# Kernel optimization log

Hardware: AMD Instinct MI355X
Metric: run time of the kernel (lower is better)

## Reference

```python
import jax, jax.numpy as jnp
import numpy as np

EPS = 1e-5  # torch BatchNorm default eps, eval mode with running stats

def _bn(x, g, b, m, v):
    shp = (1, -1) + (1,) * (x.ndim - 2)
    return (x - m.reshape(shp)) * (g.reshape(shp) / jnp.sqrt(v.reshape(shp) + EPS)) + b.reshape(shp)

def _lrelu(x):
    return jnp.where(x > 0, x, 0.2 * x)

def setup_inputs() -> dict:
    key = jax.random.key(0)
    ks = jax.random.split(key, 20)
    B, N, K = 4, 2048, 32
    Cin, Cf, Co = 6, 64, 64  # in_channels, feat_channels, out_channels(==nhiddens)
    f32 = jnp.float32
    def randn(k, shape, s=1.0):
        return jax.random.normal(k, shape, f32) * s
    def bnp(k, c):
        k1, k2, k3, k4 = jax.random.split(k, 4)
        return (randn(k1, (c,)), randn(k2, (c,)), randn(k3, (c,), 0.1),
                jax.random.uniform(k4, (c,), f32, 0.5, 1.5))
    inp = {
        "x": randn(ks[0], (B, Cin, N, K)),          # knn_points
        "y": randn(ks[1], (B, Cf, N, K)),           # knn_feat
        "points": randn(ks[2], (B, Cin // 2, N)),
        "feat": randn(ks[3], (B, Cf // 2, N)),
        "Wq": randn(ks[4], (Cf, Cf // 2), 0.1),
        "Wpos1": randn(ks[5], (Cin, Cin // 2), 0.1),
        "Wpos2": randn(ks[6], (Cf, Cin), 0.1),
        "Wattn": randn(ks[7], (Co * Cin, Cf), 0.1),
        "Wlin": randn(ks[8], (Co, Co), 0.1),
        "Wres": randn(ks[9], (Co, Cf), 0.1),
    }
    for name, k, c in [("q", ks[10], Cf), ("p", ks[11], Cin), ("a", ks[12], Co * Cin),
                       ("1", ks[13], Co), ("l", ks[14], Co), ("r", ks[15], Co)]:
        g, b, m, v = bnp(k, c)
        inp["g" + name], inp["b" + name], inp["m" + name], inp["v" + name] = g, b, m, v
    return inp

def reference(x, y, points, feat, Wq, Wpos1, Wpos2, Wattn, Wlin, Wres,
              gq, bq, mq, vq, gp, bp, mp, vp, ga, ba, ma, va,
              g1, b1, m1, v1, gl, bl, ml, vl, gr, br, mr, vr):
    B, Cin, N, K = x.shape
    Cf = y.shape[1]
    Co = Wattn.shape[0] // Cin
    # query projection (conv1d 1x1 == per-point GEMM) + BN + LeakyReLU
    x_q = _lrelu(_bn(jnp.einsum('oi,bin->bon', Wq, feat), gq, bq, mq, vq))   # [B,Cf,N]
    # positional branch
    pos = _lrelu(_bn(jnp.einsum('oi,bin->bon', Wpos1, points), gp, bp, mp, vp))  # [B,Cin,N]
    pos = pos[:, :, :, None] - x                                             # [B,Cin,N,K]
    pos = jnp.einsum('oi,bink->bonk', Wpos2, pos)                            # [B,Cf,N,K]
    # vector (subtraction) attention, softmax over neighbors k
    attn = x_q[:, :, :, None] - y + pos                                      # [B,Cf,N,K]
    attn = jax.nn.softmax(attn / float(np.sqrt(Cf)), axis=-1)
    attn = _bn(jnp.einsum('oi,bink->bonk', Wattn, attn), ga, ba, ma, va)     # [B,Co*Cin,N,K]
    # per-point tiny matmul: [Co,Cin] @ [Cin] for every (b,n,k)
    attn = attn.transpose(0, 2, 3, 1).reshape(B, N, K, Co, Cin)
    out = jnp.einsum('bnkoi,bnki->bonk', attn, x.transpose(0, 2, 3, 1))      # [B,Co,N,K]
    h = _lrelu(_bn(out, g1, b1, m1, v1))
    h = _bn(jnp.einsum('oi,bink->bonk', Wlin, h), gl, bl, ml, vl)
    res = _bn(jnp.einsum('oi,bink->bonk', Wres, y), gr, br, mr, vr)
    return _lrelu(h + res)
```

## Files before the change

### kernel.cpp

```cpp
#include <hip/hip_runtime.h>

constexpr int NB  = 4;
constexpr int NPT = 2048;
constexpr int KNN = 32;
constexpr int CIN = 6;
constexpr int CF  = 64;
constexpr int CO  = 64;
constexpr float EPS = 1e-5f;

typedef short bf16x8 __attribute__((ext_vector_type(8)));
typedef float f32x4  __attribute__((ext_vector_type(4)));

constexpr size_t WS_WA  = 0;
constexpr size_t WS_WL  = 49152;
constexpr size_t WS_WR  = 57344;
constexpr size_t WS_BA  = 65536;
constexpr size_t WS_BNF = 67072;

__device__ __host__ inline unsigned short bf16_rne(float f) {
  unsigned u = __builtin_bit_cast(unsigned, f);
  u += 0x7fffu + ((u >> 16) & 1u);
  return (unsigned short)(u >> 16);
}

__global__ void setup_kernel(const float *Wattn, const float *Wlin, const float *Wres,
                             const float *ga, const float *ba, const float *ma, const float *va,
                             const float *g1, const float *b1, const float *m1, const float *v1,
                             const float *gl, const float *bl, const float *ml, const float *vl,
                             const float *gr, const float *br, const float *mr, const float *vr,
                             unsigned short *WAf, unsigned short *WLf, unsigned short *WRf,
                             float *baP, float *bnf) {
  const int t = blockIdx.x * blockDim.x + threadIdx.x;
  const int stride = gridDim.x * blockDim.x;
  for (int e = t; e < 6 * 4 * 2 * 64 * 8; e += stride) {
    const int j = e & 7, l = (e >> 3) & 63, ks = (e >> 9) & 1, ot = (e >> 10) & 3, i = e >> 12;
    const int m = l & 15, cg = l >> 4;
    const int cc = ks * 32 + cg * 8 + j;
    const int row = (ot * 16 + m) * CIN + i;
    const float sa = ga[row] * rsqrtf(va[row] + EPS);
    WAf[e] = bf16_rne(Wattn[row * CF + cc] * sa);
  }
  for (int e = t; e < 4 * 2 * 64 * 8; e += stride) {
    const int j = e & 7, l = (e >> 3) & 63, ks = (e >> 9) & 1, ot = e >> 10;
    const int m = l & 15;
    const int cc = ks * 32 + (l >> 4) * 8 + j;
    const int row = ot * 16 + m;
    const float sl = gl[row] * rsqrtf(vl[row] + EPS);
    const float sr = gr[row] * rsqrtf(vr[row] + EPS);
    WLf[e] = bf16_rne(Wlin[row * CF + cc] * sl);
    WRf[e] = bf16_rne(Wres[row * CF + cc] * sr);
  }
  for (int e = t; e < 384; e += stride) {
    const int i = e >> 6, o = e & 63;
    const int j0 = o * CIN + i;
    const float sa = ga[j0] * rsqrtf(va[j0] + EPS);
    baP[e] = ba[j0] - ma[j0] * sa;
  }
  for (int e = t; e < 64; e += stride) {
    const float s1v = g1[e] * rsqrtf(v1[e] + EPS);
    bnf[e]      = s1v;
    bnf[64 + e] = b1[e] - m1[e] * s1v;
    const float slv = gl[e] * rsqrtf(vl[e] + EPS);
    const float srv = gr[e] * rsqrtf(vr[e] + EPS);
    bnf[128 + e] = (bl[e] - ml[e] * slv) + (br[e] - mr[e] * srv);
  }
}

struct Params {
  const float *x, *y, *points, *feat;
  const float *Wq, *Wpos1, *Wpos2;
  const float *gq, *bq, *mq, *vq;
  const float *gp, *bp, *mp, *vp;
  const unsigned short *WAf, *WLf, *WRf;
  const float *baP, *bnf;
  float *out;
};

__global__ __launch_bounds__(256) void fused_pt_attn(Params p) {
  const int tid  = threadIdx.x;
  const int lane = tid & 63;
  const int wid  = tid >> 6;
  const int bid  = ((blockIdx.x & 7) << 8) + (blockIdx.x >> 3);
  const int pidx = bid * 4 + wid;
  const int b    = pidx >> 11;
  const int n    = pidx & (NPT - 1);

  __shared__ unsigned short s_B[4][2 * 2048];
  __shared__ float s_d[4][192];
  __shared__ float s_f[4][32];
  unsigned short *yB = s_B[wid];
  unsigned short *PB = s_B[wid] + 2048;
  float *dW = s_d[wid];
  float *fW = s_f[wid];

  float ftv = 0.f, ptv = 0.f;
  if (lane < 32) ftv = p.feat[((size_t)b * 32 + lane) * NPT + n];
  if (lane < 3)  ptv = p.points[((size_t)b * 3 + lane) * NPT + n];
  const int xi = lane >> 3, xk = (lane & 7) * 4;
  float4 x4 = make_float4(0.f, 0.f, 0.f, 0.f);
  if (lane < 48)
    x4 = *(const float4 *)(p.x + (((size_t)b * CIN + xi) * NPT + n) * KNN + xk);
  const float *w2p = p.Wpos2 + lane * 6;
  const float2 w2a = *(const float2 *)(w2p);
  const float2 w2b = *(const float2 *)(w2p + 2);
  const float2 w2c = *(const float2 *)(w2p + 4);
  const float w2[6] = {w2a.x, w2a.y, w2b.x, w2b.y, w2c.x, w2c.y};

  if (lane < 32) fW[lane] = ftv;

  const float pt0 = __shfl(ptv, 0), pt1 = __shfl(ptv, 1), pt2 = __shfl(ptv, 2);
  float pos1[6];
#pragma unroll
  for (int i = 0; i < 6; ++i) {
    const float a = p.Wpos1[i * 3 + 0] * pt0 + p.Wpos1[i * 3 + 1] * pt1 +
                    p.Wpos1[i * 3 + 2] * pt2;
    const float s = p.gp[i] * rsqrtf(p.vp[i] + EPS);
    const float v = fmaf(a, s, p.bp[i] - p.mp[i] * s);
    pos1[i] = v > 0.f ? v : 0.2f * v;
  }

  if (lane < 48) {
    float pi = pos1[0];
    pi = (xi == 1) ? pos1[1] : pi;
    pi = (xi == 2) ? pos1[2] : pi;
    pi = (xi == 3) ? pos1[3] : pi;
    pi = (xi == 4) ? pos1[4] : pi;
    pi = (xi == 5) ? pos1[5] : pi;
    *(float4 *)(dW + xi * 32 + xk) =
        make_float4(pi - x4.x, pi - x4.y, pi - x4.z, pi - x4.w);
  }

  float xq;
  {
    float acc = 0.f;
    const float *wq = p.Wq + lane * 32;
#pragma unroll
    for (int q = 0; q < 8; ++q) {
      const float4 w4 = *(const float4 *)(wq + q * 4);
      const float4 f4 = *(const float4 *)(fW + q * 4);
      acc = fmaf(w4.x, f4.x, fmaf(w4.y, f4.y, fmaf(w4.z, f4.z, fmaf(w4.w, f4.w, acc))));
    }
    const float s = p.gq[lane] * rsqrtf(p.vq[lane] + EPS);
    const float v = fmaf(acc, s, p.bq[lane] - p.mq[lane] * s);
    xq = v > 0.f ? v : 0.2f * v;
  }

  float pre[32];
#pragma unroll
  for (int k = 0; k < 32; ++k) pre[k] = 0.f;
#pragma unroll
  for (int i = 0; i < 6; ++i) {
    const float wv = w2[i];
#pragma unroll
    for (int q = 0; q < 8; ++q) {
      const float4 d4 = *(const float4 *)(dW + i * 32 + q * 4);
      pre[q * 4 + 0] = fmaf(wv, d4.x, pre[q * 4 + 0]);
      pre[q * 4 + 1] = fmaf(wv, d4.y, pre[q * 4 + 1]);
      pre[q * 4 + 2] = fmaf(wv, d4.z, pre[q * 4 + 2]);
      pre[q * 4 + 3] = fmaf(wv, d4.w, pre[q * 4 + 3]);
    }
  }

  const float *yrow = p.y + (((size_t)b * CF + lane) * NPT + n) * KNN;
#pragma unroll
  for (int q = 0; q < 8; ++q) {
    const float4 y4 = *(const float4 *)(yrow + q * 4);
    const float yv[4] = {y4.x, y4.y, y4.z, y4.w};
#pragma unroll
    for (int j = 0; j < 4; ++j) {
      const int k = q * 4 + j;
      yB[k * 64 + (lane ^ ((k & 7) << 3))] = bf16_rne(yv[j]);
      pre[k] = (xq - yv[j] + pre[k]) * 0.125f;
    }
  }

  float mx = pre[0];
#pragma unroll
  for (int k = 1; k < 32; ++k) mx = fmaxf(mx, pre[k]);
  float sum = 0.f;
#pragma unroll
  for (int k = 0; k < 32; ++k) { pre[k] = __expf(pre[k] - mx); sum += pre[k]; }
  const float inv = 1.f / sum;
#pragma unroll
  for (int k = 0; k < 32; ++k)
    PB[k * 64 + (lane ^ ((k & 7) << 3))] = bf16_rne(pre[k] * inv);

  const int og = lane >> 4, kl = lane & 15;

  float xvv[6][2];
#pragma unroll
  for (int i = 0; i < 6; ++i)
#pragma unroll
    for (int nt = 0; nt < 2; ++nt)
      xvv[i][nt] = pos1[i] - dW[i * 32 + kl + nt * 16];

  bf16x8 Ba[2][2];
#pragma unroll
  for (int ks = 0; ks < 2; ++ks)
#pragma unroll
    for (int nt = 0; nt < 2; ++nt) {
      const int kcol = kl + nt * 16;
      Ba[ks][nt] = *(const bf16x8 *)(PB + kcol * 64 + ((ks * 32 + og * 8) ^ ((kcol & 7) << 3)));
    }

  const bf16x8 *WAv = (const bf16x8 *)p.WAf;
#pragma unroll
  for (int ot = 0; ot < 4; ++ot) {
    float out1[2][4] = {{0.f, 0.f, 0.f, 0.f}, {0.f, 0.f, 0.f, 0.f}};
#pragma unroll
    for (int i = 0; i < 6; ++i) {
      const bf16x8 A0 = WAv[((i * 4 + ot) * 2 + 0) * 64 + lane];
      const bf16x8 A1 = WAv[((i * 4 + ot) * 2 + 1) * 64 + lane];
      const f32x4 ba4 = *(const f32x4 *)(p.baP + i * 64 + ot * 16 + og * 4);
#pragma unroll
      for (int nt = 0; nt < 2; ++nt) {
        f32x4 g = {0.f, 0.f, 0.f, 0.f};
        g = __builtin_amdgcn_mfma_f32_16x16x32_bf16(A0, Ba[0][nt], g, 0, 0, 0);
        g = __builtin_amdgcn_mfma_f32_16x16x32_bf16(A1, Ba[1][nt], g, 0, 0, 0);
        const float xv = xvv[i][nt];
#pragma unroll
        for (int r = 0; r < 4; ++r)
          out1[nt][r] = fmaf(g[r] + ba4[r], xv, out1[nt][r]);
      }
    }
    const f32x4 s14 = *(const f32x4 *)(p.bnf + 0 * 64 + ot * 16 + og * 4);
    const f32x4 b14 = *(const f32x4 *)(p.bnf + 1 * 64 + ot * 16 + og * 4);
#pragma unroll
    for (int nt = 0; nt < 2; ++nt) {
      const int kcol = kl + nt * 16;
      unsigned hp[4];
#pragma unroll
      for (int r = 0; r < 4; ++r) {
        const float t = fmaf(s14[r], out1[nt][r], b14[r]);
        hp[r] = bf16_rne(t > 0.f ? t : 0.2f * t);
      }
      const int idx = kcol * 64 + ((ot * 16 + og * 4) ^ ((kcol & 7) << 3));
      *(uint2 *)(PB + idx) = make_uint2(hp[0] | (hp[1] << 16), hp[2] | (hp[3] << 16));
    }
  }

  bf16x8 Bh[2][2], By[2][2];
#pragma unroll
  for (int ks = 0; ks < 2; ++ks)
#pragma unroll
    for (int nt = 0; nt < 2; ++nt) {
      const int kcol = kl + nt * 16;
      const int off = kcol * 64 + ((ks * 32 + og * 8) ^ ((kcol & 7) << 3));
      Bh[ks][nt] = *(const bf16x8 *)(PB + off);
      By[ks][nt] = *(const bf16x8 *)(yB + off);
    }
  const bf16x8 *WLv = (const bf16x8 *)p.WLf;
  const bf16x8 *WRv = (const bf16x8 *)p.WRf;
#pragma unroll
  for (int ot = 0; ot < 4; ++ot) {
    const bf16x8 L0 = WLv[(ot * 2 + 0) * 64 + lane];
    const bf16x8 L1 = WLv[(ot * 2 + 1) * 64 + lane];
    const bf16x8 R0 = WRv[(ot * 2 + 0) * 64 + lane];
    const bf16x8 R1 = WRv[(ot * 2 + 1) * 64 + lane];
    const f32x4 blr = *(const f32x4 *)(p.bnf + 2 * 64 + ot * 16 + og * 4);
#pragma unroll
    for (int nt = 0; nt < 2; ++nt) {
      f32x4 a = {0.f, 0.f, 0.f, 0.f};
      a = __builtin_amdgcn_mfma_f32_16x16x32_bf16(L0, Bh[0][nt], a, 0, 0, 0);
      a = __builtin_amdgcn_mfma_f32_16x16x32_bf16(L1, Bh[1][nt], a, 0, 0, 0);
      a = __builtin_amdgcn_mfma_f32_16x16x32_bf16(R0, By[0][nt], a, 0, 0, 0);
      a = __builtin_amdgcn_mfma_f32_16x16x32_bf16(R1, By[1][nt], a, 0, 0, 0);
      const int kcol = kl + nt * 16;
      float *ob = p.out + (((size_t)(b * CO + ot * 16 + og * 4)) * NPT + n) * KNN + kcol;
#pragma unroll
      for (int r = 0; r < 4; ++r) {
        const float v = a[r] + blr[r];
        ob[(size_t)r * NPT * KNN] = v > 0.f ? v : 0.2f * v;
      }
    }
  }
}

extern "C" void kernel_launch(void *const *d_in, const int *in_sizes, int n_in,
                              void *d_out, int out_size, void *d_ws, size_t ws_size,
                              hipStream_t stream) {
  char *ws = (char *)d_ws;
  unsigned short *WAf = (unsigned short *)(ws + WS_WA);
  unsigned short *WLf = (unsigned short *)(ws + WS_WL);
  unsigned short *WRf = (unsigned short *)(ws + WS_WR);
  float *baP = (float *)(ws + WS_BA);
  float *bnf = (float *)(ws + WS_BNF);

  setup_kernel<<<dim3(96), dim3(256), 0, stream>>>(
      (const float *)d_in[7], (const float *)d_in[8], (const float *)d_in[9],
      (const float *)d_in[18], (const float *)d_in[19], (const float *)d_in[20], (const float *)d_in[21],
      (const float *)d_in[22], (const float *)d_in[23], (const float *)d_in[24], (const float *)d_in[25],
      (const float *)d_in[26], (const float *)d_in[27], (const float *)d_in[28], (const float *)d_in[29],
      (const float *)d_in[30], (const float *)d_in[31], (const float *)d_in[32], (const float *)d_in[33],
      WAf, WLf, WRf, baP, bnf);

  Params p;
  p.x      = (const float *)d_in[0];
  p.y      = (const float *)d_in[1];
  p.points = (const float *)d_in[2];
  p.feat   = (const float *)d_in[3];
  p.Wq     = (const float *)d_in[4];
  p.Wpos1  = (const float *)d_in[5];
  p.Wpos2  = (const float *)d_in[6];
  p.gq = (const float *)d_in[10]; p.bq = (const float *)d_in[11];
  p.mq = (const float *)d_in[12]; p.vq = (const float *)d_in[13];
  p.gp = (const float *)d_in[14]; p.bp = (const float *)d_in[15];
  p.mp = (const float *)d_in[16]; p.vp = (const float *)d_in[17];
  p.WAf = WAf; p.WLf = WLf; p.WRf = WRf;
  p.baP = baP; p.bnf = bnf;
  p.out = (float *)d_out;

  fused_pt_attn<<<dim3(NB * NPT / 4), dim3(256), 0, stream>>>(p);
}
```

Baseline: 66.88 us.

## Process two points per wavefront to reuse weight fragments across MFMAs

Each wavefront now handles two adjacent points instead of one, halving the grid and sharing the WA/WL/WR MFMA A-fragments and bias loads between both points. Global loads for x, y, feat and points are widened to cover both points, and y and softmax probabilities share one LDS buffer per point, with the softmax written after the y fragments are read back. It also packs the per-point x differences into bf16 pairs and sets launch_bounds occupancy to 4. Register pressure roughly doubles, and bf16 rounding of the x multiplier adds precision loss.

```diff
diff --git a/kernel.cpp b/kernel.cpp
--- a/kernel.cpp
+++ b/kernel.cpp
@@ -76,179 +76,246 @@
   float *out;
 };
 
-__global__ __launch_bounds__(256) void fused_pt_attn(Params p) {
+__global__ __launch_bounds__(256, 4) void fused_pt_attn(Params p) {
   const int tid  = threadIdx.x;
   const int lane = tid & 63;
   const int wid  = tid >> 6;
-  const int bid  = ((blockIdx.x & 7) << 8) + (blockIdx.x >> 3);
-  const int pidx = bid * 4 + wid;
-  const int b    = pidx >> 11;
-  const int n    = pidx & (NPT - 1);
-
-  __shared__ unsigned short s_B[4][2 * 2048];
-  __shared__ float s_d[4][192];
-  __shared__ float s_f[4][32];
-  unsigned short *yB = s_B[wid];
-  unsigned short *PB = s_B[wid] + 2048;
-  float *dW = s_d[wid];
-  float *fW = s_f[wid];
-
-  float ftv = 0.f, ptv = 0.f;
-  if (lane < 32) ftv = p.feat[((size_t)b * 32 + lane) * NPT + n];
-  if (lane < 3)  ptv = p.points[((size_t)b * 3 + lane) * NPT + n];
+  const int bid  = ((blockIdx.x & 7) << 7) | (blockIdx.x >> 3);
+  const int pb   = (bid * 4 + wid) * 2;
+  const int b    = pb >> 11;
+  const int n0   = pb & (NPT - 1);
+
+  __shared__ unsigned short s_BB[4][2][2048];
+  __shared__ float s_d[4][2][192];
+  __shared__ float s_f[4][2][32];
+  unsigned short *BB0 = s_BB[wid][0], *BB1 = s_BB[wid][1];
+  float *dW0 = s_d[wid][0], *dW1 = s_d[wid][1];
+  float *fW0 = s_f[wid][0], *fW1 = s_f[wid][1];
+
+  float2 ft2 = make_float2(0.f, 0.f), pt2 = make_float2(0.f, 0.f);
+  if (lane < 32) ft2 = *(const float2 *)(p.feat + ((size_t)b * 32 + lane) * NPT + n0);
+  if (lane < 3)  pt2 = *(const float2 *)(p.points + ((size_t)b * 3 + lane) * NPT + n0);
   const int xi = lane >> 3, xk = (lane & 7) * 4;
-  float4 x4 = make_float4(0.f, 0.f, 0.f, 0.f);
-  if (lane < 48)
-    x4 = *(const float4 *)(p.x + (((size_t)b * CIN + xi) * NPT + n) * KNN + xk);
+  float4 x40 = make_float4(0.f, 0.f, 0.f, 0.f), x41 = x40;
+  if (lane < 48) {
+    const float *xb = p.x + (((size_t)b * CIN + xi) * NPT + n0) * KNN + xk;
+    x40 = *(const float4 *)(xb);
+    x41 = *(const float4 *)(xb + KNN);
+  }
   const float *w2p = p.Wpos2 + lane * 6;
   const float2 w2a = *(const float2 *)(w2p);
   const float2 w2b = *(const float2 *)(w2p + 2);
   const float2 w2c = *(const float2 *)(w2p + 4);
   const float w2[6] = {w2a.x, w2a.y, w2b.x, w2b.y, w2c.x, w2c.y};
 
-  if (lane < 32) fW[lane] = ftv;
-
-  const float pt0 = __shfl(ptv, 0), pt1 = __shfl(ptv, 1), pt2 = __shfl(ptv, 2);
-  float pos1[6];
+  if (lane < 32) { fW0[lane] = ft2.x; fW1[lane] = ft2.y; }
+
+  const float pA0 = __shfl(pt2.x, 0), pA1 = __shfl(pt2.x, 1), pA2 = __shfl(pt2.x, 2);
+  const float pB0 = __shfl(pt2.y, 0), pB1 = __shfl(pt2.y, 1), pB2 = __shfl(pt2.y, 2);
+  float pos10[6], pos11[6];
 #pragma unroll
   for (int i = 0; i < 6; ++i) {
-    const float a = p.Wpos1[i * 3 + 0] * pt0 + p.Wpos1[i * 3 + 1] * pt1 +
-                    p.Wpos1[i * 3 + 2] * pt2;
-    const float s = p.gp[i] * rsqrtf(p.vp[i] + EPS);
-    const float v = fmaf(a, s, p.bp[i] - p.mp[i] * s);
-    pos1[i] = v > 0.f ? v : 0.2f * v;
+    const float w0 = p.Wpos1[i * 3 + 0], w1 = p.Wpos1[i * 3 + 1], wv = p.Wpos1[i * 3 + 2];
+    const float s  = p.gp[i] * rsqrtf(p.vp[i] + EPS);
+    const float bb = p.bp[i] - p.mp[i] * s;
+    float a0 = fmaf(w0, pA0, fmaf(w1, pA1, wv * pA2));
+    a0 = fmaf(a0, s, bb);
+    pos10[i] = a0 > 0.f ? a0 : 0.2f * a0;
+    float a1 = fmaf(w0, pB0, fmaf(w1, pB1, wv * pB2));
+    a1 = fmaf(a1, s, bb);
+    pos11[i] = a1 > 0.f ? a1 : 0.2f * a1;
   }
 
   if (lane < 48) {
-    float pi = pos1[0];
-    pi = (xi == 1) ? pos1[1] : pi;
-    pi = (xi == 2) ? pos1[2] : pi;
-    pi = (xi == 3) ? pos1[3] : pi;
-    pi = (xi == 4) ? pos1[4] : pi;
-    pi = (xi == 5) ? pos1[5] : pi;
-    *(float4 *)(dW + xi * 32 + xk) =
-        make_float4(pi - x4.x, pi - x4.y, pi - x4.z, pi - x4.w);
-  }
-
-  float xq;
+    float pi0 = pos10[0], pi1 = pos11[0];
+    pi0 = (xi == 1) ? pos10[1] : pi0;  pi1 = (xi == 1) ? pos11[1] : pi1;
+    pi0 = (xi == 2) ? pos10[2] : pi0;  pi1 = (xi == 2) ? pos11[2] : pi1;
+    pi0 = (xi == 3) ? pos10[3] : pi0;  pi1 = (xi == 3) ? pos11[3] : pi1;
+    pi0 = (xi == 4) ? pos10[4] : pi0;  pi1 = (xi == 4) ? pos11[4] : pi1;
+    pi0 = (xi == 5) ? pos10[5] : pi0;  pi1 = (xi == 5) ? pos11[5] : pi1;
+    *(float4 *)(dW0 + xi * 32 + xk) = make_float4(pi0 - x40.x, pi0 - x40.y, pi0 - x40.z, pi0 - x40.w);
+    *(float4 *)(dW1 + xi * 32 + xk) = make_float4(pi1 - x41.x, pi1 - x41.y, pi1 - x41.z, pi1 - x41.w);
+  }
+
+  float xq0, xq1;
   {
-    float acc = 0.f;
+    float a0 = 0.f, a1 = 0.f;
     const float *wq = p.Wq + lane * 32;
 #pragma unroll
     for (int q = 0; q < 8; ++q) {
       const float4 w4 = *(const float4 *)(wq + q * 4);
-      const float4 f4 = *(const float4 *)(fW + q * 4);
-      acc = fmaf(w4.x, f4.x, fmaf(w4.y, f4.y, fmaf(w4.z, f4.z, fmaf(w4.w, f4.w, acc))));
-    }
-    const float s = p.gq[lane] * rsqrtf(p.vq[lane] + EPS);
-    const float v = fmaf(acc, s, p.bq[lane] - p.mq[lane] * s);
-    xq = v > 0.f ? v : 0.2f * v;
-  }
-
-  float pre[32];
-#pragma unroll
-  for (int k = 0; k < 32; ++k) pre[k] = 0.f;
+      const float4 f0 = *(const float4 *)(fW0 + q * 4);
+      const float4 f1 = *(const float4 *)(fW1 + q * 4);
+      a0 = fmaf(w4.x, f0.x, fmaf(w4.y, f0.y, fmaf(w4.z, f0.z, fmaf(w4.w, f0.w, a0))));
+      a1 = fmaf(w4.x, f1.x, fmaf(w4.y, f1.y, fmaf(w4.z, f1.z, fmaf(w4.w, f1.w, a1))));
+    }
+    const float s  = p.gq[lane] * rsqrtf(p.vq[lane] + EPS);
+    const float bb = p.bq[lane] - p.mq[lane] * s;
+    const float v0 = fmaf(a0, s, bb), v1 = fmaf(a1, s, bb);
+    xq0 = v0 > 0.f ? v0 : 0.2f * v0;
+    xq1 = v1 > 0.f ? v1 : 0.2f * v1;
+  }
+
+  float pre0[32], pre1[32];
+#pragma unroll
+  for (int k = 0; k < 32; ++k) { pre0[k] = 0.f; pre1[k] = 0.f; }
 #pragma unroll
   for (int i = 0; i < 6; ++i) {
     const float wv = w2[i];
 #pragma unroll
     for (int q = 0; q < 8; ++q) {
-      const float4 d4 = *(const float4 *)(dW + i * 32 + q * 4);
-      pre[q * 4 + 0] = fmaf(wv, d4.x, pre[q * 4 + 0]);
-      pre[q * 4 + 1] = fmaf(wv, d4.y, pre[q * 4 + 1]);
-      pre[q * 4 + 2] = fmaf(wv, d4.z, pre[q * 4 + 2]);
-      pre[q * 4 + 3] = fmaf(wv, d4.w, pre[q * 4 + 3]);
-    }
-  }
-
-  const float *yrow = p.y + (((size_t)b * CF + lane) * NPT + n) * KNN;
+      const float4 d0 = *(const float4 *)(dW0 + i * 32 + q * 4);
+      const float4 d1 = *(const float4 *)(dW1 + i * 32 + q * 4);
+      pre0[q * 4 + 0] = fmaf(wv, d0.x, pre0[q * 4 + 0]);
+      pre0[q * 4 + 1] = fmaf(wv, d0.y, pre0[q * 4 + 1]);
+      pre0[q * 4 + 2] = fmaf(wv, d0.z, pre0[q * 4 + 2]);
+      pre0[q * 4 + 3] = fmaf(wv, d0.w, pre0[q * 4 + 3]);
+      pre1[q * 4 + 0] = fmaf(wv, d1.x, pre1[q * 4 + 0]);
+      pre1[q * 4 + 1] = fmaf(wv, d1.y, pre1[q * 4 + 1]);
+      pre1[q * 4 + 2] = fmaf(wv, d1.z, pre1[q * 4 + 2]);
+      pre1[q * 4 + 3] = fmaf(wv, d1.w, pre1[q * 4 + 3]);
+    }
+  }
+
+  const float *yrow0 = p.y + (((size_t)b * CF + lane) * NPT + n0) * KNN;
 #pragma unroll
   for (int q = 0; q < 8; ++q) {
-    const float4 y4 = *(const float4 *)(yrow + q * 4);
-    const float yv[4] = {y4.x, y4.y, y4.z, y4.w};
+    const float4 y0 = *(const float4 *)(yrow0 + q * 4);
+    const float4 y1 = *(const float4 *)(yrow0 + KNN + q * 4);
+    const float yv0[4] = {y0.x, y0.y, y0.z, y0.w};
+    const float yv1[4] = {y1.x, y1.y, y1.z, y1.w};
 #pragma unroll
     for (int j = 0; j < 4; ++j) {
       const int k = q * 4 + j;
-      yB[k * 64 + (lane ^ ((k & 7) << 3))] = bf16_rne(yv[j]);
-      pre[k] = (xq - yv[j] + pre[k]) * 0.125f;
-    }
-  }
-
-  float mx = pre[0];
-#pragma unroll
-  for (int k = 1; k < 32; ++k) mx = fmaxf(mx, pre[k]);
-  float sum = 0.f;
-#pragma unroll
-  for (int k = 0; k < 32; ++k) { pre[k] = __expf(pre[k] - mx); sum += pre[k]; }
-  const float inv = 1.f / sum;
-#pragma unroll
-  for (int k = 0; k < 32; ++k)
-    PB[k * 64 + (lane ^ ((k & 7) << 3))] = bf16_rne(pre[k] * inv);
+      const int idx = k * 64 + (lane ^ ((k & 7) << 3));
+      BB0[idx] = bf16_rne(yv0[j]);
+      BB1[idx] = bf16_rne(yv1[j]);
+      pre0[k] = (xq0 - yv0[j] + pre0[k]) * 0.125f;
+      pre1[k] = (xq1 - yv1[j] + pre1[k]) * 0.125f;
+    }
+  }
 
   const int og = lane >> 4, kl = lane & 15;
 
-  float xvv[6][2];
-#pragma unroll
-  for (int i = 0; i < 6; ++i)
-#pragma unroll
-    for (int nt = 0; nt < 2; ++nt)
-      xvv[i][nt] = pos1[i] - dW[i * 32 + kl + nt * 16];
-
-  bf16x8 Ba[2][2];
+  bf16x8 By0[2][2], By1[2][2];
 #pragma unroll
   for (int ks = 0; ks < 2; ++ks)
 #pragma unroll
     for (int nt = 0; nt < 2; ++nt) {
       const int kcol = kl + nt * 16;
-      Ba[ks][nt] = *(const bf16x8 *)(PB + kcol * 64 + ((ks * 32 + og * 8) ^ ((kcol & 7) << 3)));
-    }
+      const int off = kcol * 64 + ((ks * 32 + og * 8) ^ ((kl & 7) << 3));
+      By0[ks][nt] = *(const bf16x8 *)(BB0 + off);
+      By1[ks][nt] = *(const bf16x8 *)(BB1 + off);
+    }
+
+  {
+    float mx0 = pre0[0], mx1 = pre1[0];
+#pragma unroll
+    for (int k = 1; k < 32; ++k) { mx0 = fmaxf(mx0, pre0[k]); mx1 = fmaxf(mx1, pre1[k]); }
+    float s0 = 0.f, s1 = 0.f;
+#pragma unroll
+    for (int k = 0; k < 32; ++k) {
+      pre0[k] = __expf(pre0[k] - mx0); s0 += pre0[k];
+      pre1[k] = __expf(pre1[k] - mx1); s1 += pre1[k];
+    }
+    const float i0 = 1.f / s0, i1 = 1.f / s1;
+#pragma unroll
+    for (int k = 0; k < 32; ++k) {
+      const int idx = k * 64 + (lane ^ ((k & 7) << 3));
+      BB0[idx] = bf16_rne(pre0[k] * i0);
+      BB1[idx] = bf16_rne(pre1[k] * i1);
+    }
+  }
+
+  bf16x8 Ba0[2][2], Ba1[2][2];
+#pragma unroll
+  for (int ks = 0; ks < 2; ++ks)
+#pragma unroll
+    for (int nt = 0; nt < 2; ++nt) {
+      const int kcol = kl + nt * 16;
+      const int off = kcol * 64 + ((ks * 32 + og * 8) ^ ((kl & 7) << 3));
+      Ba0[ks][nt] = *(const bf16x8 *)(BB0 + off);
+      Ba1[ks][nt] = *(const bf16x8 *)(BB1 + off);
+    }
+
+  unsigned xvp0[6], xvp1[6];
+#pragma unroll
+  for (int i = 0; i < 6; ++i) {
+    const float a0 = pos10[i] - dW0[i * 32 + kl];
+    const float c0 = pos10[i] - dW0[i * 32 + kl + 16];
+    const float a1 = pos11[i] - dW1[i * 32 + kl];
+    const float c1 = pos11[i] - dW1[i * 32 + kl + 16];
+    xvp0[i] = (unsigned)bf16_rne(a0) | ((unsigned)bf16_rne(c0) << 16);
+    xvp1[i] = (unsigned)bf16_rne(a1) | ((unsigned)bf16_rne(c1) << 16);
+  }
 
   const bf16x8 *WAv = (const bf16x8 *)p.WAf;
 #pragma unroll
   for (int ot = 0; ot < 4; ++ot) {
-    float out1[2][4] = {{0.f, 0.f, 0.f, 0.f}, {0.f, 0.f, 0.f, 0.f}};
+    f32x4 o00 = {0.f, 0.f, 0.f, 0.f}, o01 = o00, o10 = o00, o11 = o00;
 #pragma unroll
     for (int i = 0; i < 6; ++i) {
       const bf16x8 A0 = WAv[((i * 4 + ot) * 2 + 0) * 64 + lane];
       const bf16x8 A1 = WAv[((i * 4 + ot) * 2 + 1) * 64 + lane];
       const f32x4 ba4 = *(const f32x4 *)(p.baP + i * 64 + ot * 16 + og * 4);
-#pragma unroll
-      for (int nt = 0; nt < 2; ++nt) {
-        f32x4 g = {0.f, 0.f, 0.f, 0.f};
-        g = __builtin_amdgcn_mfma_f32_16x16x32_bf16(A0, Ba[0][nt], g, 0, 0, 0);
-        g = __builtin_amdgcn_mfma_f32_16x16x32_bf16(A1, Ba[1][nt], g, 0, 0, 0);
-        const float xv = xvv[i][nt];
-#pragma unroll
-        for (int r = 0; r < 4; ++r)
-          out1[nt][r] = fmaf(g[r] + ba4[r], xv, out1[nt][r]);
-      }
+      const float xv00 = __builtin_bit_cast(float, xvp0[i] << 16);
+      const float xv01 = __builtin_bit_cast(float, xvp0[i] & 0xffff0000u);
+      const float xv10 = __builtin_bit_cast(float, xvp1[i] << 16);
+      const float xv11 = __builtin_bit_cast(float, xvp1[i] & 0xffff0000u);
+      f32x4 g;
+      g = (f32x4){0.f, 0.f, 0.f, 0.f};
+      g = __builtin_amdgcn_mfma_f32_16x16x32_bf16(A0, Ba0[0][0], g, 0, 0, 0);
+      g = __builtin_amdgcn_mfma_f32_16x16x32_bf16(A1, Ba0[1][0], g, 0, 0, 0);
+#pragma unroll
+      for (int r = 0; r < 4; ++r) o00[r] = fmaf(g[r] + ba4[r], xv00, o00[r]);
+      g = (f32x4){0.f, 0.f, 0.f, 0.f};
+      g = __builtin_amdgcn_mfma_f32_16x16x32_bf16(A0, Ba0[0][1], g, 0, 0, 0);
+      g = __builtin_amdgcn_mfma_f32_16x16x32_bf16(A1, Ba0[1][1], g, 0, 0, 0);
+#pragma unroll
+      for (int r = 0; r < 4; ++r) o01[r] = fmaf(g[r] + ba4[r], xv01, o01[r]);
+      g = (f32x4){0.f, 0.f, 0.f, 0.f};
+      g = __builtin_amdgcn_mfma_f32_16x16x32_bf16(A0, Ba1[0][0], g, 0, 0, 0);
+      g = __builtin_amdgcn_mfma_f32_16x16x32_bf16(A1, Ba1[1][0], g, 0, 0, 0);
+#pragma unroll
+      for (int r = 0; r < 4; ++r) o10[r] = fmaf(g[r] + ba4[r], xv10, o10[r]);
+      g = (f32x4){0.f, 0.f, 0.f, 0.f};
+      g = __builtin_amdgcn_mfma_f32_16x16x32_bf16(A0, Ba1[0][1], g, 0, 0, 0);
+      g = __builtin_amdgcn_mfma_f32_16x16x32_bf16(A1, Ba1[1][1], g, 0, 0, 0);
+#pragma unroll
+      for (int r = 0; r < 4; ++r) o11[r] = fmaf(g[r] + ba4[r], xv11, o11[r]);
     }
     const f32x4 s14 = *(const f32x4 *)(p.bnf + 0 * 64 + ot * 16 + og * 4);
     const f32x4 b14 = *(const f32x4 *)(p.bnf + 1 * 64 + ot * 16 + og * 4);
 #pragma unroll
     for (int nt = 0; nt < 2; ++nt) {
       const int kcol = kl + nt * 16;
-      unsigned hp[4];
+      const int idx = kcol * 64 + ((ot * 16 + og * 4) ^ ((kl & 7) << 3));
+      const f32x4 &q0 = nt ? o01 : o00;
+      const f32x4 &q1 = nt ? o11 : o10;
+      unsigned h0[4], h1[4];
 #pragma unroll
       for (int r = 0; r < 4; ++r) {
-        const float t = fmaf(s14[r], out1[nt][r], b14[r]);
-        hp[r] = bf16_rne(t > 0.f ? t : 0.2f * t);
+        const float t0 = fmaf(s14[r], q0[r], b14[r]);
+        const float t1 = fmaf(s14[r], q1[r], b14[r]);
+        h0[r] = bf16_rne(t0 > 0.f ? t0 : 0.2f * t0);
+        h1[r] = bf16_rne(t1 > 0.f ? t1 : 0.2f * t1);
       }
-      const int idx = kcol * 64 + ((ot * 16 + og * 4) ^ ((kcol & 7) << 3));
-      *(uint2 *)(PB + idx) = make_uint2(hp[0] | (hp[1] << 16), hp[2] | (hp[3] << 16));
-    }
-  }
-
-  bf16x8 Bh[2][2], By[2][2];
+      *(uint2 *)(BB0 + idx) = make_uint2(h0[0] | (h0[1] << 16), h0[2] | (h0[3] << 16));
+      *(uint2 *)(BB1 + idx) = make_uint2(h1[0] | (h1[1] << 16), h1[2] | (h1[3] << 16));
+    }
+  }
+
+  bf16x8 Bh0[2][2], Bh1[2][2];
 #pragma unroll
   for (int ks = 0; ks < 2; ++ks)
 #pragma unroll
     for (int nt = 0; nt < 2; ++nt) {
       const int kcol = kl + nt * 16;
-      const int off = kcol * 64 + ((ks * 32 + og * 8) ^ ((kcol & 7) << 3));
-      Bh[ks][nt] = *(const bf16x8 *)(PB + off);
-      By[ks][nt] = *(const bf16x8 *)(yB + off);
-    }
+      const int off = kcol * 64 + ((ks * 32 + og * 8) ^ ((kl & 7) << 3));
+      Bh0[ks][nt] = *(const bf16x8 *)(BB0 + off);
+      Bh1[ks][nt] = *(const bf16x8 *)(BB1 + off);
+    }
+
   const bf16x8 *WLv = (const bf16x8 *)p.WLf;
   const bf16x8 *WRv = (const bf16x8 *)p.WRf;
 #pragma unroll
@@ -260,17 +327,23 @@
     const f32x4 blr = *(const f32x4 *)(p.bnf + 2 * 64 + ot * 16 + og * 4);
 #pragma unroll
     for (int nt = 0; nt < 2; ++nt) {
-      f32x4 a = {0.f, 0.f, 0.f, 0.f};
-      a = __builtin_amdgcn_mfma_f32_16x16x32_bf16(L0, Bh[0][nt], a, 0, 0, 0);
-      a = __builtin_amdgcn_mfma_f32_16x16x32_bf16(L1, Bh[1][nt], a, 0, 0, 0);
-      a = __builtin_amdgcn_mfma_f32_16x16x32_bf16(R0, By[0][nt], a, 0, 0, 0);
-      a = __builtin_amdgcn_mfma_f32_16x16x32_bf16(R1, By[1][nt], a, 0, 0, 0);
-      const int kcol = kl + nt * 16;
-      float *ob = p.out + (((size_t)(b * CO + ot * 16 + og * 4)) * NPT + n) * KNN + kcol;
+      f32x4 a0 = {0.f, 0.f, 0.f, 0.f}, a1 = a0;
+      a0 = __builtin_amdgcn_mfma_f32_16x16x32_bf16(L0, Bh0[0][nt], a0, 0, 0, 0);
+      a0 = __builtin_amdgcn_mfma_f32_16x16x32_bf16(L1, Bh0[1][nt], a0, 0, 0, 0);
+      a0 = __builtin_amdgcn_mfma_f32_16x16x32_bf16(R0, By0[0][nt], a0, 0, 0, 0);
+      a0 = __builtin_amdgcn_mfma_f32_16x16x32_bf16(R1, By0[1][nt], a0, 0, 0, 0);
+      a1 = __builtin_amdgcn_mfma_f32_16x16x32_bf16(L0, Bh1[0][nt], a1, 0, 0, 0);
+      a1 = __builtin_amdgcn_mfma_f32_16x16x32_bf16(L1, Bh1[1][nt], a1, 0, 0, 0);
+      a1 = __builtin_amdgcn_mfma_f32_16x16x32_bf16(R0, By1[0][nt], a1, 0, 0, 0);
+      a1 = __builtin_amdgcn_mfma_f32_16x16x32_bf16(R1, By1[1][nt], a1, 0, 0, 0);
+      const int kcol = kl + nt * 16;
+      float *ob = p.out + (((size_t)(b * CO + ot * 16 + og * 4)) * NPT + n0) * KNN + kcol;
 #pragma unroll
       for (int r = 0; r < 4; ++r) {
-        const float v = a[r] + blr[r];
-        ob[(size_t)r * NPT * KNN] = v > 0.f ? v : 0.2f * v;
+        const float v0 = a0[r] + blr[r];
+        const float v1 = a1[r] + blr[r];
+        ob[(size_t)r * NPT * KNN]       = v0 > 0.f ? v0 : 0.2f * v0;
+        ob[(size_t)r * NPT * KNN + KNN] = v1 > 0.f ? v1 : 0.2f * v1;
       }
     }
   }
@@ -310,5 +383,5 @@
   p.baP = baP; p.bnf = bnf;
   p.out = (float *)d_out;
 
-  fused_pt_attn<<<dim3(NB * NPT / 4), dim3(256), 0, stream>>>(p);
+  fused_pt_attn<<<dim3(NB * NPT / 8), dim3(256), 0, stream>>>(p);
 }
```

Result: slower. 119.0 us (+78.0%).

## Split output-channel tiles across waves and keep attention weights in registers

Applied to the files above, without the earlier changes.

Each block now handles 8 points in two iterations. Instead of every wave computing all 64 output channels for its own point, each wave owns one 16-channel tile and loops over the four points staged in shared memory. This lets each wave hold its slice of the large attention weight matrix in registers once, rather than reloading all of it from global memory per point. The cost is several block-wide barriers per iteration, cross-wave shared-memory traffic, extra shared arrays for x, and higher register pressure with a launch-bounds occupancy hint.

```diff
diff --git a/kernel.cpp b/kernel.cpp
--- a/kernel.cpp
+++ b/kernel.cpp
@@ -76,201 +76,230 @@
   float *out;
 };
 
-__global__ __launch_bounds__(256) void fused_pt_attn(Params p) {
+__global__ __launch_bounds__(256, 4) void fused_pt_attn(Params p) {
   const int tid  = threadIdx.x;
   const int lane = tid & 63;
-  const int wid  = tid >> 6;
-  const int bid  = ((blockIdx.x & 7) << 8) + (blockIdx.x >> 3);
-  const int pidx = bid * 4 + wid;
-  const int b    = pidx >> 11;
-  const int n    = pidx & (NPT - 1);
-
-  __shared__ unsigned short s_B[4][2 * 2048];
+  const int wv   = tid >> 6;
+  const int bid  = ((blockIdx.x & 7) << 7) | (blockIdx.x >> 3);
+  const int p0   = bid * 8;
+  const int b    = p0 >> 11;
+  const int nb0  = p0 & (NPT - 1);
+
+  __shared__ unsigned short s_P[4][2048];
+  __shared__ unsigned short s_Y[4][2048];
+  __shared__ float s_x[4][192];
   __shared__ float s_d[4][192];
   __shared__ float s_f[4][32];
-  unsigned short *yB = s_B[wid];
-  unsigned short *PB = s_B[wid] + 2048;
-  float *dW = s_d[wid];
-  float *fW = s_f[wid];
-
-  float ftv = 0.f, ptv = 0.f;
-  if (lane < 32) ftv = p.feat[((size_t)b * 32 + lane) * NPT + n];
-  if (lane < 3)  ptv = p.points[((size_t)b * 3 + lane) * NPT + n];
-  const int xi = lane >> 3, xk = (lane & 7) * 4;
-  float4 x4 = make_float4(0.f, 0.f, 0.f, 0.f);
-  if (lane < 48)
-    x4 = *(const float4 *)(p.x + (((size_t)b * CIN + xi) * NPT + n) * KNN + xk);
+
+  const int og = lane >> 4, kl = lane & 15;
+  const int swz = (kl & 7) << 3;
+
+  const bf16x8 *WAv = (const bf16x8 *)p.WAf;
+  bf16x8 WA[6][2];
+#pragma unroll
+  for (int i = 0; i < 6; ++i)
+#pragma unroll
+    for (int ks = 0; ks < 2; ++ks)
+      WA[i][ks] = WAv[((i * 4 + wv) * 2 + ks) * 64 + lane];
+
   const float *w2p = p.Wpos2 + lane * 6;
   const float2 w2a = *(const float2 *)(w2p);
   const float2 w2b = *(const float2 *)(w2p + 2);
   const float2 w2c = *(const float2 *)(w2p + 4);
   const float w2[6] = {w2a.x, w2a.y, w2b.x, w2b.y, w2c.x, w2c.y};
 
-  if (lane < 32) fW[lane] = ftv;
-
-  const float pt0 = __shfl(ptv, 0), pt1 = __shfl(ptv, 1), pt2 = __shfl(ptv, 2);
-  float pos1[6];
-#pragma unroll
-  for (int i = 0; i < 6; ++i) {
-    const float a = p.Wpos1[i * 3 + 0] * pt0 + p.Wpos1[i * 3 + 1] * pt1 +
-                    p.Wpos1[i * 3 + 2] * pt2;
-    const float s = p.gp[i] * rsqrtf(p.vp[i] + EPS);
-    const float v = fmaf(a, s, p.bp[i] - p.mp[i] * s);
-    pos1[i] = v > 0.f ? v : 0.2f * v;
-  }
-
-  if (lane < 48) {
-    float pi = pos1[0];
-    pi = (xi == 1) ? pos1[1] : pi;
-    pi = (xi == 2) ? pos1[2] : pi;
-    pi = (xi == 3) ? pos1[3] : pi;
-    pi = (xi == 4) ? pos1[4] : pi;
-    pi = (xi == 5) ? pos1[5] : pi;
-    *(float4 *)(dW + xi * 32 + xk) =
-        make_float4(pi - x4.x, pi - x4.y, pi - x4.z, pi - x4.w);
-  }
-
-  float xq;
-  {
-    float acc = 0.f;
-    const float *wq = p.Wq + lane * 32;
-#pragma unroll
-    for (int q = 0; q < 8; ++q) {
-      const float4 w4 = *(const float4 *)(wq + q * 4);
-      const float4 f4 = *(const float4 *)(fW + q * 4);
-      acc = fmaf(w4.x, f4.x, fmaf(w4.y, f4.y, fmaf(w4.z, f4.z, fmaf(w4.w, f4.w, acc))));
+  for (int it = 0; it < 2; ++it) {
+    __syncthreads();
+
+    {
+      const int n = nb0 + it * 4 + wv;
+      unsigned short *PB = s_P[wv];
+      unsigned short *YB = s_Y[wv];
+      float *dW = s_d[wv], *xW = s_x[wv], *fW = s_f[wv];
+
+      float ftv = 0.f, ptv = 0.f;
+      if (lane < 32) ftv = p.feat[((size_t)b * 32 + lane) * NPT + n];
+      if (lane < 3)  ptv = p.points[((size_t)b * 3 + lane) * NPT + n];
+      const int xi = lane >> 3, xk = (lane & 7) * 4;
+      float4 x4 = make_float4(0.f, 0.f, 0.f, 0.f);
+      if (lane < 48)
+        x4 = *(const float4 *)(p.x + (((size_t)b * CIN + xi) * NPT + n) * KNN + xk);
+
+      if (lane < 32) fW[lane] = ftv;
+
+      const float pt0 = __shfl(ptv, 0), pt1 = __shfl(ptv, 1), pt2 = __shfl(ptv, 2);
+      float pos1[6];
+#pragma unroll
+      for (int i = 0; i < 6; ++i) {
+        const float a = p.Wpos1[i * 3 + 0] * pt0 + p.Wpos1[i * 3 + 1] * pt1 +
+                        p.Wpos1[i * 3 + 2] * pt2;
+        const float s = p.gp[i] * rsqrtf(p.vp[i] + EPS);
+        const float v = fmaf(a, s, p.bp[i] - p.mp[i] * s);
+        pos1[i] = v > 0.f ? v : 0.2f * v;
+      }
+
+      if (lane < 48) {
+        float pi = pos1[0];
+        pi = (xi == 1) ? pos1[1] : pi;
+        pi = (xi == 2) ? pos1[2] : pi;
+        pi = (xi == 3) ? pos1[3] : pi;
+        pi = (xi == 4) ? pos1[4] : pi;
+        pi = (xi == 5) ? pos1[5] : pi;
+        *(float4 *)(dW + xi * 32 + xk) =
+            make_float4(pi - x4.x, pi - x4.y, pi - x4.z, pi - x4.w);
+        *(float4 *)(xW + xi * 32 + xk) = x4;
+      }
+
+      float xq;
+      {
+        float acc = 0.f;
+        const float *wq = p.Wq + lane * 32;
+#pragma unroll
+        for (int q = 0; q < 8; ++q) {
+          const float4 w4 = *(const float4 *)(wq + q * 4);
+          const float4 f4 = *(const float4 *)(fW + q * 4);
+          acc = fmaf(w4.x, f4.x, fmaf(w4.y, f4.y, fmaf(w4.z, f4.z, fmaf(w4.w, f4.w, acc))));
+        }
+        const float s = p.gq[lane] * rsqrtf(p.vq[lane] + EPS);
+        const float v = fmaf(acc, s, p.bq[lane] - p.mq[lane] * s);
+        xq = v > 0.f ? v : 0.2f * v;
+      }
+
+      float pre[32];
+#pragma unroll
+      for (int k = 0; k < 32; ++k) pre[k] = 0.f;
+#pragma unroll
+      for (int i = 0; i < 6; ++i) {
+        const float wvv = w2[i];
+#pragma unroll
+        for (int q = 0; q < 8; ++q) {
+          const float4 d4 = *(const float4 *)(dW + i * 32 + q * 4);
+          pre[q * 4 + 0] = fmaf(wvv, d4.x, pre[q * 4 + 0]);
+          pre[q * 4 + 1] = fmaf(wvv, d4.y, pre[q * 4 + 1]);
+          pre[q * 4 + 2] = fmaf(wvv, d4.z, pre[q * 4 + 2]);
+          pre[q * 4 + 3] = fmaf(wvv, d4.w, pre[q * 4 + 3]);
+        }
+      }
+
+      const float *yrow = p.y + (((size_t)b * CF + lane) * NPT + n) * KNN;
+#pragma unroll
+      for (int q = 0; q < 8; ++q) {
+        const float4 y4 = *(const float4 *)(yrow + q * 4);
+        const float yv[4] = {y4.x, y4.y, y4.z, y4.w};
+#pragma unroll
+        for (int j = 0; j < 4; ++j) {
+          const int k = q * 4 + j;
+          YB[k * 64 + (lane ^ ((k & 7) << 3))] = bf16_rne(yv[j]);
+          pre[k] = (xq - yv[j] + pre[k]) * 0.125f;
+        }
+      }
+
+      float mx = pre[0];
+#pragma unroll
+      for (int k = 1; k < 32; ++k) mx = fmaxf(mx, pre[k]);
+      float sum = 0.f;
+#pragma unroll
+      for (int k = 0; k < 32; ++k) { pre[k] = __expf(pre[k] - mx); sum += pre[k]; }
+      const float inv = 1.f / sum;
+#pragma unroll
+      for (int k = 0; k < 32; ++k)
+        PB[k * 64 + (lane ^ ((k & 7) << 3))] = bf16_rne(pre[k] * inv);
     }
-    const float s = p.gq[lane] * rsqrtf(p.vq[lane] + EPS);
-    const float v = fmaf(acc, s, p.bq[lane] - p.mq[lane] * s);
-    xq = v > 0.f ? v : 0.2f * v;
-  }
-
-  float pre[32];
-#pragma unroll
-  for (int k = 0; k < 32; ++k) pre[k] = 0.f;
-#pragma unroll
-  for (int i = 0; i < 6; ++i) {
-    const float wv = w2[i];
-#pragma unroll
-    for (int q = 0; q < 8; ++q) {
-      const float4 d4 = *(const float4 *)(dW + i * 32 + q * 4);
-      pre[q * 4 + 0] = fmaf(wv, d4.x, pre[q * 4 + 0]);
-      pre[q * 4 + 1] = fmaf(wv, d4.y, pre[q * 4 + 1]);
-      pre[q * 4 + 2] = fmaf(wv, d4.z, pre[q * 4 + 2]);
-      pre[q * 4 + 3] = fmaf(wv, d4.w, pre[q * 4 + 3]);
+    __syncthreads();
+
+    uint2 hp[4][2];
+    {
+      const f32x4 s14 = *(const f32x4 *)(p.bnf + 0 * 64 + wv * 16 + og * 4);
+      const f32x4 b14 = *(const f32x4 *)(p.bnf + 1 * 64 + wv * 16 + og * 4);
+#pragma unroll
+      for (int qq = 0; qq < 4; ++qq) {
+        const int q = (qq + wv) & 3;
+        const unsigned short *Pq = s_P[q];
+        const float *xWq = s_x[q];
+        bf16x8 Ba[2][2];
+#pragma unroll
+        for (int ks = 0; ks < 2; ++ks)
+#pragma unroll
+          for (int nt = 0; nt < 2; ++nt)
+            Ba[ks][nt] = *(const bf16x8 *)(Pq + (kl + nt * 16) * 64 +
+                                           ((ks * 32 + og * 8) ^ swz));
+        f32x4 o0 = {0.f, 0.f, 0.f, 0.f}, o1 = o0;
+#pragma unroll
+        for (int i = 0; i < 6; ++i) {
+          const f32x4 ba4 = *(const f32x4 *)(p.baP + i * 64 + wv * 16 + og * 4);
+          const float xv0 = xWq[i * 32 + kl];
+          const float xv1 = xWq[i * 32 + kl + 16];
+          f32x4 g = {0.f, 0.f, 0.f, 0.f};
+          g = __builtin_amdgcn_mfma_f32_16x16x32_bf16(WA[i][0], Ba[0][0], g, 0, 0, 0);
+          g = __builtin_amdgcn_mfma_f32_16x16x32_bf16(WA[i][1], Ba[1][0], g, 0, 0, 0);
+#pragma unroll
+          for (int r = 0; r < 4; ++r) o0[r] = fmaf(g[r] + ba4[r], xv0, o0[r]);
+          g = (f32x4){0.f, 0.f, 0.f, 0.f};
+          g = __builtin_amdgcn_mfma_f32_16x16x32_bf16(WA[i][0], Ba[0][1], g, 0, 0, 0);
+          g = __builtin_amdgcn_mfma_f32_16x16x32_bf16(WA[i][1], Ba[1][1], g, 0, 0, 0);
+#pragma unroll
+          for (int r = 0; r < 4; ++r) o1[r] = fmaf(g[r] + ba4[r], xv1, o1[r]);
+        }
+#pragma unroll
+        for (int nt = 0; nt < 2; ++nt) {
+          const f32x4 &oo = nt ? o1 : o0;
+          unsigned hb[4];
+#pragma unroll
+          for (int r = 0; r < 4; ++r) {
+            const float t = fmaf(s14[r], oo[r], b14[r]);
+            hb[r] = bf16_rne(t > 0.f ? t : 0.2f * t);
+          }
+          hp[qq][nt] = make_uint2(hb[0] | (hb[1] << 16), hb[2] | (hb[3] << 16));
+        }
+      }
     }
-  }
-
-  const float *yrow = p.y + (((size_t)b * CF + lane) * NPT + n) * KNN;
-#pragma unroll
-  for (int q = 0; q < 8; ++q) {
-    const float4 y4 = *(const float4 *)(yrow + q * 4);
-    const float yv[4] = {y4.x, y4.y, y4.z, y4.w};
-#pragma unroll
-    for (int j = 0; j < 4; ++j) {
-      const int k = q * 4 + j;
-      yB[k * 64 + (lane ^ ((k & 7) << 3))] = bf16_rne(yv[j]);
-      pre[k] = (xq - yv[j] + pre[k]) * 0.125f;
+    __syncthreads();
+
+#pragma unroll
+    for (int qq = 0; qq < 4; ++qq) {
+      const int q = (qq + wv) & 3;
+      unsigned short *Pq = s_P[q];
+#pragma unroll
+      for (int nt = 0; nt < 2; ++nt)
+        *(uint2 *)(Pq + (kl + nt * 16) * 64 + ((wv * 16 + og * 4) ^ swz)) = hp[qq][nt];
     }
-  }
-
-  float mx = pre[0];
-#pragma unroll
-  for (int k = 1; k < 32; ++k) mx = fmaxf(mx, pre[k]);
-  float sum = 0.f;
-#pragma unroll
-  for (int k = 0; k < 32; ++k) { pre[k] = __expf(pre[k] - mx); sum += pre[k]; }
-  const float inv = 1.f / sum;
-#pragma unroll
-  for (int k = 0; k < 32; ++k)
-    PB[k * 64 + (lane ^ ((k & 7) << 3))] = bf16_rne(pre[k] * inv);
-
-  const int og = lane >> 4, kl = lane & 15;
-
-  float xvv[6][2];
-#pragma unroll
-  for (int i = 0; i < 6; ++i)
-#pragma unroll
-    for (int nt = 0; nt < 2; ++nt)
-      xvv[i][nt] = pos1[i] - dW[i * 32 + kl + nt * 16];
-
-  bf16x8 Ba[2][2];
-#pragma unroll
-  for (int ks = 0; ks < 2; ++ks)
-#pragma unroll
-    for (int nt = 0; nt < 2; ++nt) {
-      const int kcol = kl + nt * 16;
-      Ba[ks][nt] = *(const bf16x8 *)(PB + kcol * 64 + ((ks * 32 + og * 8) ^ ((kcol & 7) << 3)));
-    }
-
-  const bf16x8 *WAv = (const bf16x8 *)p.WAf;
-#pragma unroll
-  for (int ot = 0; ot < 4; ++ot) {
-    float out1[2][4] = {{0.f, 0.f, 0.f, 0.f}, {0.f, 0.f, 0.f, 0.f}};
-#pragma unroll
-    for (int i = 0; i < 6; ++i) {
-      const bf16x8 A0 = WAv[((i * 4 + ot) * 2 + 0) * 64 + lane];
-      const bf16x8 A1 = WAv[((i * 4 + ot) * 2 + 1) * 64 + lane];
-      const f32x4 ba4 = *(const f32x4 *)(p.baP + i * 64 + ot * 16 + og * 4);
-#pragma unroll
-      for (int nt = 0; nt < 2; ++nt) {
-        f32x4 g = {0.f, 0.f, 0.f, 0.f};
-        g = __builtin_amdgcn_mfma_f32_16x16x32_bf16(A0, Ba[0][nt], g, 0, 0, 0);
-        g = __builtin_amdgcn_mfma_f32_16x16x32_bf16(A1, Ba[1][nt], g, 0, 0, 0);
-        const float xv = xvv[i][nt];
-#pragma unroll
-        for (int r = 0; r < 4; ++r)
-          out1[nt][r] = fmaf(g[r] + ba4[r], xv, out1[nt][r]);
-      }
-    }
-    const f32x4 s14 = *(const f32x4 *)(p.bnf + 0 * 64 + ot * 16 + og * 4);
-    const f32x4 b14 = *(const f32x4 *)(p.bnf + 1 * 64 + ot * 16 + og * 4);
-#pragma unroll
-    for (int nt = 0; nt < 2; ++nt) {
-      const int kcol = kl + nt * 16;
-      unsigned hp[4];
-#pragma unroll
-      for (int r = 0; r < 4; ++r) {
-        const float t = fmaf(s14[r], out1[nt][r], b14[r]);
-        hp[r] = bf16_rne(t > 0.f ? t : 0.2f * t);
-      }
-      const int idx = kcol * 64 + ((ot * 16 + og * 4) ^ ((kcol & 7) << 3));
-      *(uint2 *)(PB + idx) = make_uint2(hp[0] | (hp[1] << 16), hp[2] | (hp[3] << 16));
-    }
-  }
-
-  bf16x8 Bh[2][2], By[2][2];
-#pragma unroll
-  for (int ks = 0; ks < 2; ++ks)
-#pragma unroll
-    for (int nt = 0; nt < 2; ++nt) {
-      const int kcol = kl + nt * 16;
-      const int off = kcol * 64 + ((ks * 32 + og * 8) ^ ((kcol & 7) << 3));
-      Bh[ks][nt] = *(const bf16x8 *)(PB + off);
-      By[ks][nt] = *(const bf16x8 *)(yB + off);
-    }
-  const bf16x8 *WLv = (const bf16x8 *)p.WLf;
-  const bf16x8 *WRv = (const bf16x8 *)p.WRf;
-#pragma unroll
-  for (int ot = 0; ot < 4; ++ot) {
-    const bf16x8 L0 = WLv[(ot * 2 + 0) * 64 + lane];
-    const bf16x8 L1 = WLv[(ot * 2 + 1) * 64 + lane];
-    const bf16x8 R0 = WRv[(ot * 2 + 0) * 64 + lane];
-    const bf16x8 R1 = WRv[(ot * 2 + 1) * 64 + lane];
-    const f32x4 blr = *(const f32x4 *)(p.bnf + 2 * 64 + ot * 16 + og * 4);
-#pragma unroll
-    for (int nt = 0; nt < 2; ++nt) {
-      f32x4 a = {0.f, 0.f, 0.f, 0.f};
-      a = __builtin_amdgcn_mfma_f32_16x16x32_bf16(L0, Bh[0][nt], a, 0, 0, 0);
-      a = __builtin_amdgcn_mfma_f32_16x16x32_bf16(L1, Bh[1][nt], a, 0, 0, 0);
-      a = __builtin_amdgcn_mfma_f32_16x16x32_bf16(R0, By[0][nt], a, 0, 0, 0);
-      a = __builtin_amdgcn_mfma_f32_16x16x32_bf16(R1, By[1][nt], a, 0, 0, 0);
-      const int kcol = kl + nt * 16;
-      float *ob = p.out + (((size_t)(b * CO + ot * 16 + og * 4)) * NPT + n) * KNN + kcol;
-#pragma unroll
-      for (int r = 0; r < 4; ++r) {
-        const float v = a[r] + blr[r];
-        ob[(size_t)r * NPT * KNN] = v > 0.f ? v : 0.2f * v;
+    __syncthreads();
+
+    {
+      const bf16x8 *WLv = (const bf16x8 *)p.WLf;
+      const bf16x8 *WRv = (const bf16x8 *)p.WRf;
+      const bf16x8 L0 = WLv[(wv * 2 + 0) * 64 + lane];
+      const bf16x8 L1 = WLv[(wv * 2 + 1) * 64 + lane];
+      const bf16x8 R0 = WRv[(wv * 2 + 0) * 64 + lane];
+      const bf16x8 R1 = WRv[(wv * 2 + 1) * 64 + lane];
+      const f32x4 blr = *(const f32x4 *)(p.bnf + 2 * 64 + wv * 16 + og * 4);
+#pragma unroll
+      for (int qq = 0; qq < 4; ++qq) {
+        const int q = (qq + wv) & 3;
+        const int nq = nb0 + it * 4 + q;
+        const unsigned short *Pq = s_P[q];
+        const unsigned short *Yq = s_Y[q];
+#pragma unroll
+        for (int nt = 0; nt < 2; ++nt) {
+          const int off0 = (kl + nt * 16) * 64 + ((0 * 32 + og * 8) ^ swz);
+          const int off1 = (kl + nt * 16) * 64 + ((1 * 32 + og * 8) ^ swz);
+          const bf16x8 Bh0 = *(const bf16x8 *)(Pq + off0);
+          const bf16x8 Bh1 = *(const bf16x8 *)(Pq + off1);
+          const bf16x8 By0 = *(const bf16x8 *)(Yq + off0);
+          const bf16x8 By1 = *(const bf16x8 *)(Yq + off1);
+          f32x4 a = {0.f, 0.f, 0.f, 0.f};
+          a = __builtin_amdgcn_mfma_f32_16x16x32_bf16(L0, Bh0, a, 0, 0, 0);
+          a = __builtin_amdgcn_mfma_f32_16x16x32_bf16(L1, Bh1, a, 0, 0, 0);
+          a = __builtin_amdgcn_mfma_f32_16x16x32_bf16(R0, By0, a, 0, 0, 0);
+          a = __builtin_amdgcn_mfma_f32_16x16x32_bf16(R1, By1, a, 0, 0, 0);
+          float *ob = p.out + (((size_t)(b * CO + wv * 16 + og * 4)) * NPT + nq) * KNN +
+                      kl + nt * 16;
+#pragma unroll
+          for (int r = 0; r < 4; ++r) {
+            const float v = a[r] + blr[r];
+            ob[(size_t)r * NPT * KNN] = v > 0.f ? v : 0.2f * v;
+          }
+        }
       }
     }
   }
@@ -310,5 +339,5 @@
   p.baP = baP; p.bnf = bnf;
   p.out = (float *)d_out;
 
-  fused_pt_attn<<<dim3(NB * NPT / 4), dim3(256), 0, stream>>>(p);
+  fused_pt_attn<<<dim3(NB * NPT / 8), dim3(256), 0, stream>>>(p);
 }
```

Measured after the change: 158.7 us. 137% more time.
